# Optimization experiments

Measured on AMD Instinct MI355X. Metric: run time of the kernel, lower is better.

## Reference

```python
import jax, jax.numpy as jnp
import numpy as np

NEG_SLOPE = 0.2
EPS = 1e-9


def setup_inputs() -> dict:
    key = jax.random.key(0)
    ks = jax.random.split(key, 6)
    B, N, E, H, F = 2, 40000, 640000, 4, 32
    X = jax.random.normal(ks[0], (B, N, H, F), dtype=jnp.float32)
    A_self = jax.random.normal(ks[1], (H, F), dtype=jnp.float32)
    A_adjc = jax.random.normal(ks[2], (H, F), dtype=jnp.float32)
    targets = jax.random.randint(ks[3], (B, E), 0, N, dtype=jnp.int32)
    sources = jax.random.randint(ks[4], (B, E), 0, N, dtype=jnp.int32)
    degree = jax.random.uniform(ks[5], (B, E), dtype=jnp.float32)
    return {"X": X, "A_self": A_self, "A_adjc": A_adjc, "degree": degree,
            "targets": targets, "sources": sources, "N": N}


def reference(X, A_self, A_adjc, degree, targets, sources, N):
    # X: [B, N, H, F]; targets/sources: [B, E]
    # per-node attention logits: [B, N, H]
    e_self = jnp.einsum("bnhf,hf->bnh", X, A_self)
    e_adjc = jnp.einsum("bnhf,hf->bnh", X, A_adjc)
    # gather to edges: [B, E, H]
    es = jnp.take_along_axis(e_self, targets[:, :, None], axis=1)
    ea = jnp.take_along_axis(e_adjc, sources[:, :, None], axis=1)
    e = jax.nn.leaky_relu(es + ea, negative_slope=NEG_SLOPE)

    seg_max = jax.vmap(lambda v, i: jax.ops.segment_max(v, i, num_segments=N))
    seg_sum = jax.vmap(lambda v, i: jax.ops.segment_sum(v, i, num_segments=N))

    # exact normalization from source: exp(e - seg_max(e)), then divide by
    # seg_max of the exponentials (+eps), both gathered back to edges.
    m1 = jnp.take_along_axis(seg_max(e, targets), targets[:, :, None], axis=1)
    e = jnp.exp(e - m1)
    m2 = jnp.take_along_axis(seg_max(e, targets), targets[:, :, None], axis=1)
    attn = (e / (m2 + EPS))[..., None]  # [B, E, H, 1]; dropout omitted (eval)

    # message passing: gather source features, weight, scatter-sum to targets
    msg = jnp.take_along_axis(X, sources[:, :, None, None], axis=1) * attn  # [B,E,H,F]
    out = seg_sum(msg, targets)  # [B, N, H, F]
    return out
```

## Files before the change

### kernel.cpp

```cpp
#include <hip/hip_runtime.h>
#include <stdint.h>

#define BB     2
#define NNODE  40000
#define NEDGE  640000
#define NH     4
#define NF     32
#define NHF    128
#define SEGN   (BB * NNODE)
#define GEDGE  (BB * NEDGE)
#define EC     16
#define SLOT   48

#define W      512
#define NBK_B  79
#define NBK    (BB * NBK_B)
#define CAP    9216
#define BLK_E  2048
#define NBLKA  (GEDGE / BLK_E)

static constexpr float NEG_SLOPE = 0.2f;
static constexpr float NEG_BIG   = -3.4e38f;

__global__ void prep_k(const float* __restrict__ X,
                       const float* __restrict__ As,
                       const float* __restrict__ Aa,
                       float* __restrict__ S, float* __restrict__ A,
                       unsigned* __restrict__ cursor) {
    int idx = blockIdx.x * blockDim.x + threadIdx.x;
    if (idx < NBK) cursor[idx] = 0u;
    if (idx >= SEGN * NH) return;
    int h = idx & (NH - 1);
    const float4* xv = (const float4*)(X + (size_t)idx * NF);
    const float4* sv = (const float4*)(As + h * NF);
    const float4* av = (const float4*)(Aa + h * NF);
    float s = 0.f, a = 0.f;
#pragma unroll
    for (int i = 0; i < 8; ++i) {
        float4 x = xv[i];
        float4 ws = sv[i];
        float4 wa = av[i];
        s += x.x * ws.x + x.y * ws.y + x.z * ws.z + x.w * ws.w;
        a += x.x * wa.x + x.y * wa.y + x.z * wa.z + x.w * wa.w;
    }
    S[idx] = s;
    A[idx] = a;
}

__global__ __launch_bounds__(256) void binA_k(const int* __restrict__ tg,
                                              const int* __restrict__ sc,
                                              unsigned* __restrict__ cursor,
                                              unsigned* __restrict__ pairs) {
    __shared__ unsigned hist[NBK];
    __shared__ unsigned lofs[NBK];
    __shared__ unsigned gofs[NBK];
    __shared__ unsigned staged[BLK_E];
    __shared__ unsigned char sbk[BLK_E];
    int t = threadIdx.x;
    int base = blockIdx.x * BLK_E;
    for (int i = t; i < NBK; i += 256) hist[i] = 0u;
    __syncthreads();

    unsigned pr[8];
    unsigned short pbk[8], plp[8];
#pragma unroll
    for (int k = 0; k < 8; ++k) {
        int e = base + k * 256 + t;
        int tgv = tg[e], scv = sc[e];
        int b = (e >= NEDGE) ? 1 : 0;
        unsigned bk = (unsigned)(b * NBK_B + (tgv >> 9));
        pr[k]  = ((unsigned)(tgv & (W - 1)) << 16) | (unsigned)scv;
        pbk[k] = (unsigned short)bk;
        plp[k] = (unsigned short)atomicAdd(&hist[bk], 1u);
    }
    __syncthreads();
    if (t == 0) {
        unsigned run = 0;
        for (int i = 0; i < NBK; ++i) { lofs[i] = run; run += hist[i]; }
    }
    __syncthreads();
    if (t < NBK && hist[t] > 0u)
        gofs[t] = atomicAdd(&cursor[t], hist[t]);
    __syncthreads();
#pragma unroll
    for (int k = 0; k < 8; ++k) {
        unsigned j = lofs[pbk[k]] + plp[k];
        staged[j] = pr[k];
        sbk[j] = (unsigned char)pbk[k];
    }
    __syncthreads();
    for (int j = t; j < BLK_E; j += 256) {
        unsigned bk = sbk[j];
        unsigned dst = gofs[bk] + ((unsigned)j - lofs[bk]);
        if (dst < CAP)
            pairs[(size_t)bk * CAP + dst] = staged[j];
    }
}

__global__ __launch_bounds__(256) void binB_k(const unsigned* __restrict__ cursor,
                                              const unsigned* __restrict__ pairs,
                                              unsigned short* __restrict__ srt,
                                              unsigned* __restrict__ deg) {
    __shared__ unsigned short loc[W * SLOT];
    __shared__ unsigned dloc[W];
    int t = threadIdx.x;
    int gbk = blockIdx.x;
    int b = gbk / NBK_B;
    int bkloc = gbk - b * NBK_B;
    int node0 = b * NNODE + bkloc * W;
    int wEff = min(W, NNODE - bkloc * W);
    for (int i = t; i < W; i += 256) dloc[i] = 0u;
    __syncthreads();
    int nE = (int)min(cursor[gbk], (unsigned)CAP);
    const unsigned* pb = pairs + (size_t)gbk * CAP;
    for (int j = t; j < nE; j += 256) {
        unsigned p = pb[j];
        unsigned tl = p >> 16;
        unsigned pos = atomicAdd(&dloc[tl], 1u);
        if (pos < SLOT)
            loc[tl * SLOT + pos] = (unsigned short)(p & 0xFFFFu);
    }
    __syncthreads();
    unsigned* srt32 = (unsigned*)(srt + (size_t)node0 * SLOT);
    const unsigned* loc32 = (const unsigned*)loc;
    int n32 = wEff * SLOT / 2;
    for (int i = t; i < n32; i += 256) srt32[i] = loc32[i];
    for (int i = t; i < wEff; i += 256) deg[node0 + i] = dloc[i];
}

__global__ __launch_bounds__(64) void gather_k(
        const float* __restrict__ X, const float* __restrict__ S,
        const float* __restrict__ A, const unsigned* __restrict__ deg,
        const unsigned short* __restrict__ srt, float* __restrict__ OUT) {
    int node = blockIdx.x;
    int t = threadIdx.x;
    int hs = t & 3;
    int es = t >> 2;
    int ha = t >> 4;
    int dg = min((int)deg[node], SLOT);
    int bbase = (node >= NNODE) ? NNODE : 0;
    size_t beg = (size_t)node * SLOT;

    float sh = S[node * NH + hs];
    float m_st = NEG_BIG;
    float m_ac = NEG_BIG;
    float ax = 0.f, ay = 0.f;

    for (int c = 0; c < dg; c += EC) {
        int e = c + es;
        int sb = bbase;
        float v = NEG_BIG;
        if (e < dg) {
            sb = bbase + (int)srt[beg + e];
            v = sh + A[sb * NH + hs];
            v = v > 0.f ? v : NEG_SLOPE * v;
        }
        float m = v;
        m = fmaxf(m, __shfl_xor(m, 4));
        m = fmaxf(m, __shfl_xor(m, 8));
        m = fmaxf(m, __shfl_xor(m, 16));
        m = fmaxf(m, __shfl_xor(m, 32));
        m_st = fmaxf(m_st, m);
        float w = (e < dg) ? __expf(v - m_st) : 0.f;
        float ma_new = fmaxf(m_ac, __shfl(m, ha));
        float r = __expf(m_ac - ma_new);
        m_ac = ma_new;
        ax *= r; ay *= r;

        int cend = min(EC, dg - c);
#pragma unroll 8
        for (int e2 = 0; e2 < cend; ++e2) {
            float we  = __shfl(w, 4 * e2 + ha);
            int   sbe = __shfl(sb, 4 * e2);
            const float2 x = *(const float2*)(X + (size_t)sbe * NHF + 2 * t);
            ax += x.x * we;
            ay += x.y * we;
        }
    }
    float2* o = (float2*)(OUT + (size_t)node * NHF + 2 * t);
    *o = make_float2(ax, ay);
}

extern "C" void kernel_launch(void* const* d_in, const int* in_sizes, int n_in,
                              void* d_out, int out_size, void* d_ws, size_t ws_size,
                              hipStream_t stream) {
    const float* X  = (const float*)d_in[0];
    const float* As = (const float*)d_in[1];
    const float* Aa = (const float*)d_in[2];
    const int* tg = (const int*)d_in[4];
    const int* sc = (const int*)d_in[5];
    float* OUT = (float*)d_out;

    char* ws = (char*)d_ws;
    float*          S      = (float*)ws;
    float*          A      = (float*)(ws + 1280000);
    unsigned*       deg    = (unsigned*)(ws + 2560000);
    unsigned*       cursor = (unsigned*)(ws + 2880000);
    unsigned*       pairs  = (unsigned*)(ws + 2880640);
    unsigned short* srt    = (unsigned short*)(ws + 8705152);

    const int nlog = SEGN * NH;
    prep_k<<<(nlog + 255) / 256, 256, 0, stream>>>(X, As, Aa, S, A, cursor);
    binA_k<<<NBLKA, 256, 0, stream>>>(tg, sc, cursor, pairs);
    binB_k<<<NBK, 256, 0, stream>>>(cursor, pairs, srt, deg);
    gather_k<<<SEGN, 64, 0, stream>>>(X, S, A, deg, srt, OUT);
}
```

Baseline: 238.2 us.

## Parallel scan in binning, wider binB blocks, float4 two-edge gather

Replaces the single-thread serial prefix over bucket histograms in binA with a wave shuffle scan plus cross-wave offsets. binB_k runs with 1024 threads per block. gather_k packs four nodes per 256-thread block and has each half-wave handle alternate edges with float4 loads, then combines the halves with a shuffle. This targets serialization in the scan and low memory-level parallelism in the gather, at the cost of an extra reduction and more registers per thread.

```diff
diff --git a/kernel.cpp b/kernel.cpp
--- a/kernel.cpp
+++ b/kernel.cpp
@@ -54,6 +54,7 @@
     __shared__ unsigned hist[NBK];
     __shared__ unsigned lofs[NBK];
     __shared__ unsigned gofs[NBK];
+    __shared__ unsigned wsum[4];
     __shared__ unsigned staged[BLK_E];
     __shared__ unsigned char sbk[BLK_E];
     int t = threadIdx.x;
@@ -74,13 +75,26 @@
         plp[k] = (unsigned short)atomicAdd(&hist[bk], 1u);
     }
     __syncthreads();
-    if (t == 0) {
-        unsigned run = 0;
-        for (int i = 0; i < NBK; ++i) { lofs[i] = run; run += hist[i]; }
-    }
-    __syncthreads();
-    if (t < NBK && hist[t] > 0u)
-        gofs[t] = atomicAdd(&cursor[t], hist[t]);
+    {
+        int lane = t & 63, w = t >> 6;
+        unsigned v = (t < NBK) ? hist[t] : 0u;
+        unsigned inc = v;
+#pragma unroll
+        for (int d = 1; d < 64; d <<= 1) {
+            unsigned u = __shfl_up(inc, d);
+            if (lane >= d) inc += u;
+        }
+        if (lane == 63) wsum[w] = inc;
+        __syncthreads();
+        unsigned woff = 0;
+#pragma unroll
+        for (int i = 0; i < 3; ++i) { if (i < w) woff += wsum[i]; }
+        if (t < NBK) {
+            lofs[t] = woff + inc - v;
+            if (v > 0u)
+                gofs[t] = atomicAdd(&cursor[t], v);
+        }
+    }
     __syncthreads();
 #pragma unroll
     for (int k = 0; k < 8; ++k) {
@@ -97,10 +111,10 @@
     }
 }
 
-__global__ __launch_bounds__(256) void binB_k(const unsigned* __restrict__ cursor,
-                                              const unsigned* __restrict__ pairs,
-                                              unsigned short* __restrict__ srt,
-                                              unsigned* __restrict__ deg) {
+__global__ __launch_bounds__(1024) void binB_k(const unsigned* __restrict__ cursor,
+                                               const unsigned* __restrict__ pairs,
+                                               unsigned short* __restrict__ srt,
+                                               unsigned* __restrict__ deg) {
     __shared__ unsigned short loc[W * SLOT];
     __shared__ unsigned dloc[W];
     int t = threadIdx.x;
@@ -109,11 +123,11 @@
     int bkloc = gbk - b * NBK_B;
     int node0 = b * NNODE + bkloc * W;
     int wEff = min(W, NNODE - bkloc * W);
-    for (int i = t; i < W; i += 256) dloc[i] = 0u;
+    for (int i = t; i < W; i += 1024) dloc[i] = 0u;
     __syncthreads();
     int nE = (int)min(cursor[gbk], (unsigned)CAP);
     const unsigned* pb = pairs + (size_t)gbk * CAP;
-    for (int j = t; j < nE; j += 256) {
+    for (int j = t; j < nE; j += 1024) {
         unsigned p = pb[j];
         unsigned tl = p >> 16;
         unsigned pos = atomicAdd(&dloc[tl], 1u);
@@ -124,19 +138,21 @@
     unsigned* srt32 = (unsigned*)(srt + (size_t)node0 * SLOT);
     const unsigned* loc32 = (const unsigned*)loc;
     int n32 = wEff * SLOT / 2;
-    for (int i = t; i < n32; i += 256) srt32[i] = loc32[i];
-    for (int i = t; i < wEff; i += 256) deg[node0 + i] = dloc[i];
-}
-
-__global__ __launch_bounds__(64) void gather_k(
+    for (int i = t; i < n32; i += 1024) srt32[i] = loc32[i];
+    for (int i = t; i < wEff; i += 1024) deg[node0 + i] = dloc[i];
+}
+
+__global__ __launch_bounds__(256) void gather_k(
         const float* __restrict__ X, const float* __restrict__ S,
         const float* __restrict__ A, const unsigned* __restrict__ deg,
         const unsigned short* __restrict__ srt, float* __restrict__ OUT) {
-    int node = blockIdx.x;
-    int t = threadIdx.x;
+    int node = blockIdx.x * 4 + (threadIdx.x >> 6);
+    int t = threadIdx.x & 63;
     int hs = t & 3;
     int es = t >> 2;
-    int ha = t >> 4;
+    int h32 = t >> 5;
+    int q = t & 31;
+    int haq = q >> 3;
     int dg = min((int)deg[node], SLOT);
     int bbase = (node >= NNODE) ? NNODE : 0;
     size_t beg = (size_t)node * SLOT;
@@ -144,7 +160,7 @@
     float sh = S[node * NH + hs];
     float m_st = NEG_BIG;
     float m_ac = NEG_BIG;
-    float ax = 0.f, ay = 0.f;
+    float4 acc = make_float4(0.f, 0.f, 0.f, 0.f);
 
     for (int c = 0; c < dg; c += EC) {
         int e = c + es;
@@ -162,23 +178,33 @@
         m = fmaxf(m, __shfl_xor(m, 32));
         m_st = fmaxf(m_st, m);
         float w = (e < dg) ? __expf(v - m_st) : 0.f;
-        float ma_new = fmaxf(m_ac, __shfl(m, ha));
+        float ma_new = fmaxf(m_ac, __shfl(m, haq));
         float r = __expf(m_ac - ma_new);
         m_ac = ma_new;
-        ax *= r; ay *= r;
+        acc.x *= r; acc.y *= r; acc.z *= r; acc.w *= r;
 
         int cend = min(EC, dg - c);
+        int npair = (cend + 1) >> 1;
 #pragma unroll 8
-        for (int e2 = 0; e2 < cend; ++e2) {
-            float we  = __shfl(w, 4 * e2 + ha);
+        for (int i = 0; i < npair; ++i) {
+            int e2 = 2 * i + h32;
+            float we  = __shfl(w, 4 * e2 + haq);
             int   sbe = __shfl(sb, 4 * e2);
-            const float2 x = *(const float2*)(X + (size_t)sbe * NHF + 2 * t);
-            ax += x.x * we;
-            ay += x.y * we;
-        }
-    }
-    float2* o = (float2*)(OUT + (size_t)node * NHF + 2 * t);
-    *o = make_float2(ax, ay);
+            const float4 x = *(const float4*)(X + (size_t)sbe * NHF + 4 * q);
+            acc.x += x.x * we;
+            acc.y += x.y * we;
+            acc.z += x.z * we;
+            acc.w += x.w * we;
+        }
+    }
+    acc.x += __shfl_xor(acc.x, 32);
+    acc.y += __shfl_xor(acc.y, 32);
+    acc.z += __shfl_xor(acc.z, 32);
+    acc.w += __shfl_xor(acc.w, 32);
+    if (t < 32) {
+        float4* o = (float4*)(OUT + (size_t)node * NHF + 4 * q);
+        *o = acc;
+    }
 }
 
 extern "C" void kernel_launch(void* const* d_in, const int* in_sizes, int n_in,
@@ -202,6 +228,6 @@
     const int nlog = SEGN * NH;
     prep_k<<<(nlog + 255) / 256, 256, 0, stream>>>(X, As, Aa, S, A, cursor);
     binA_k<<<NBLKA, 256, 0, stream>>>(tg, sc, cursor, pairs);
-    binB_k<<<NBK, 256, 0, stream>>>(cursor, pairs, srt, deg);
-    gather_k<<<SEGN, 64, 0, stream>>>(X, S, A, deg, srt, OUT);
-}
+    binB_k<<<NBK, 1024, 0, stream>>>(cursor, pairs, srt, deg);
+    gather_k<<<SEGN / 4, 256, 0, stream>>>(X, S, A, deg, srt, OUT);
+}
```

After: 221.0 us. -7.2%, faster.
